# Kernel tuning notes

Hardware: AMD Instinct MI355X
Metric: run time of the kernel (lower is better)

Reference implementation:

```python
import jax, jax.numpy as jnp
import numpy as np

NUM_SEGMENTS = 4096  # number of graphs in the batch


def setup_inputs() -> dict:
    key = jax.random.key(0)
    k1, k2, k3, k4, k5, k6 = jax.random.split(key, 6)
    N, H = 1048576, 128
    x = jax.random.normal(k1, (N, H), dtype=jnp.float32)
    batch = jnp.sort(jax.random.randint(k2, (N,), 0, NUM_SEGMENTS, dtype=jnp.int64))
    # Linear params, PyTorch layout: W [out, in], b [out]
    W1 = jax.random.normal(k3, (2 * H, H), dtype=jnp.float32) * (1.0 / np.sqrt(H))
    b1 = jax.random.normal(k4, (2 * H,), dtype=jnp.float32) * 0.01
    W2 = jax.random.normal(k5, (H, 2 * H), dtype=jnp.float32) * (1.0 / np.sqrt(2 * H))
    b2 = jax.random.normal(k6, (H,), dtype=jnp.float32) * 0.01
    return {"x": x, "batch": batch, "W1": W1, "b1": b1, "W2": W2, "b2": b2}


def reference(x, batch, W1, b1, W2, b2):
    # phi(x) = tanh(fc1(x))  -> [N, 2H]
    phi_x = jnp.tanh(jnp.einsum('nh,oh->no', x, W1) + b1)
    # scatter-sum pooling per graph -> [G, 2H]
    sum_x = jax.ops.segment_sum(phi_x, batch, num_segments=NUM_SEGMENTS)
    # fc2 -> [G, H]; .squeeze() is a no-op for these shapes
    y = jnp.einsum('go,ho->gh', sum_x, W2) + b2
    return jnp.squeeze(y)
```

## Files before the change

### kernel.cpp

```cpp
#include <hip/hip_runtime.h>
#include <hip/hip_bf16.h>

#define NTOT 1048576
#define NSEG 4096
#define HDIM 128
#define ODIM 256
#define GRID1 2048
#define NSTEP 8

typedef __attribute__((ext_vector_type(8))) short bf16x8;
typedef __attribute__((ext_vector_type(4))) float f32x4;
typedef __attribute__((ext_vector_type(4))) unsigned int u32x4;

__device__ __forceinline__ unsigned int cvt_pk(float lo, float hi) {
    unsigned int r;
    asm("v_cvt_pk_bf16_f32 %0, %1, %2" : "=v"(r) : "v"(lo), "v"(hi));
    return r;
}

__global__ void zero_convert(const float* __restrict__ W1, unsigned int* __restrict__ W1b,
                             float* __restrict__ sumx) {
    int gid = blockIdx.x * 256 + threadIdx.x;
    sumx[gid] = 0.0f;
    if (gid < (ODIM * HDIM / 2)) {
        float2 v = *(const float2*)(W1 + 2 * gid);
        W1b[gid] = cvt_pk(v.x, v.y);
    }
}

__global__ __launch_bounds__(256, 2)
void stage1(const float* __restrict__ x, const int* __restrict__ batch,
            const unsigned short* __restrict__ W1b, const float* __restrict__ b1,
            float* __restrict__ sumx) {
    __shared__ __align__(16) unsigned char w1s[ODIM * HDIM * 2];

    const int t    = threadIdx.x;
    const int lane = t & 63;
    const int wv   = t >> 6;
    const int l15  = lane & 15;
    const int lhi  = (lane >> 4) & 3;

    const bool is64 = (batch[NTOT - 1] == 0);

    for (int c = t; c < 4096; c += 256) {
        u32x4 v = ((const u32x4*)W1b)[c];
        int row = c >> 4;
        int kb  = (c & 15) * 16;
        *(u32x4*)(w1s + row * 256 + (kb ^ ((row & 7) << 4))) = v;
    }
    float bias[16];
    #pragma unroll
    for (int nf = 0; nf < 16; ++nf) bias[nf] = b1[nf * 16 + l15];
    __syncthreads();

    int lra[4];
    #pragma unroll
    for (int ks = 0; ks < 4; ++ks)
        lra[ks] = l15 * 256 + ((ks * 64 + lhi * 16) ^ ((l15 & 7) << 4));

    const long rowbase = (long)blockIdx.x * 512 + (long)wv * 128;
    const char* xrow = (const char*)x + (rowbase + l15) * 512 + lhi * 32;

    int curSeg = batch[is64 ? 2 * rowbase : rowbase];
    float runsum[16];
    #pragma unroll
    for (int nf = 0; nf < 16; ++nf) runsum[nf] = 0.f;

#define FLUSH()                                                                  \
    do { if (lhi == 0) {                                                         \
            float* _b = sumx + (long)curSeg * ODIM + l15;                        \
            _Pragma("unroll")                                                    \
            for (int nf = 0; nf < 16; ++nf) atomicAdd(_b + nf * 16, runsum[nf]); \
        }                                                                        \
        _Pragma("unroll")                                                        \
        for (int nf = 0; nf < 16; ++nf) runsum[nf] = 0.f;                        \
    } while (0)

#define LOADSTEP(dst, s)                                                          \
    do { const char* _p = xrow + (size_t)(s) * 8192;                              \
        _Pragma("unroll")                                                         \
        for (int ks = 0; ks < 4; ++ks) {                                          \
            dst[2*ks]   = *(const f32x4*)(_p + ks * 128);                         \
            dst[2*ks+1] = *(const f32x4*)(_p + ks * 128 + 16);                    \
        }                                                                         \
    } while (0)

#define STEP(s, cur, nxt)                                                         \
    do {                                                                          \
        if ((s) + 1 < NSTEP) LOADSTEP(nxt, (s) + 1);    \
        const long _r0 = rowbase + (long)(s) * 16;                                \
        int seg_l = batch[is64 ? 2 * (_r0 + l15) : (_r0 + l15)];                  \
        int prv   = __shfl(seg_l, lane > 0 ? lane - 1 : 0);                       \
        unsigned bm = (unsigned)(__ballot(seg_l != prv)) & 0xFFFEu;               \
        int seg0 = __shfl(seg_l, 0);                                              \
        f32x4 acc[16];                                                            \
        _Pragma("unroll")                                                         \
        for (int nf = 0; nf < 16; ++nf)                                           \
            acc[nf] = (f32x4){bias[nf], bias[nf], bias[nf], bias[nf]};            \
        _Pragma("unroll")                                                         \
        for (int ks = 0; ks < 4; ++ks) {                                          \
            u32x4 w;                                                              \
            w.x = cvt_pk(cur[2*ks].x,   cur[2*ks].y);                             \
            w.y = cvt_pk(cur[2*ks].z,   cur[2*ks].w);                             \
            w.z = cvt_pk(cur[2*ks+1].x, cur[2*ks+1].y);                           \
            w.w = cvt_pk(cur[2*ks+1].z, cur[2*ks+1].w);                           \
            bf16x8 af = __builtin_bit_cast(bf16x8, w);                            \
            _Pragma("unroll")                                                     \
            for (int nf = 0; nf < 16; ++nf) {                                     \
                bf16x8 bf = *(const bf16x8*)(w1s + lra[ks] + nf * 4096);          \
                acc[nf] = __builtin_amdgcn_mfma_f32_16x16x32_bf16(af, bf, acc[nf], 0, 0, 0); \
            }                                                                     \
        }                                                                         \
        _Pragma("unroll")                                                         \
        for (int nf = 0; nf < 16; ++nf)                                           \
            _Pragma("unroll")                                                     \
            for (int r = 0; r < 4; ++r) {                                         \
                float e = exp2f(acc[nf][r] * 2.885390081777927f);                 \
                acc[nf][r] = 1.0f - 2.0f * __builtin_amdgcn_rcpf(1.0f + e);       \
            }                                                                     \
        if (seg0 != curSeg) { FLUSH(); curSeg = seg0; }                           \
        int start = 0;                                                            \
        unsigned rem = bm;                                                        \
        for (;;) {                                                                \
            const int end = rem ? (int)__builtin_ctz(rem) : 16;                   \
            _Pragma("unroll")                                                     \
            for (int nf = 0; nf < 16; ++nf) {                                     \
                float sp = 0.f;                                                   \
                _Pragma("unroll")                                                 \
                for (int r = 0; r < 4; ++r) {                                     \
                    int row = lhi * 4 + r;                                        \
                    float wgt = ((unsigned)(row - start) < (unsigned)(end - start)) ? 1.0f : 0.0f; \
                    sp = fmaf(wgt, acc[nf][r], sp);                               \
                }                                                                 \
                sp += __shfl_xor(sp, 16);                                         \
                sp += __shfl_xor(sp, 32);                                         \
                runsum[nf] += sp;                                                 \
            }                                                                     \
            if (end == 16) break;                                                 \
            FLUSH();                                                              \
            curSeg = __shfl(seg_l, end);                                          \
            rem &= rem - 1;                                                       \
            start = end;                                                          \
        }                                                                         \
    } while (0)

    f32x4 cA[8], cB[8];
    LOADSTEP(cA, 0);
    #pragma unroll
    for (int s = 0; s < NSTEP; s += 2) {
        STEP(s, cA, cB);
        STEP(s + 1, cB, cA);
    }
    FLUSH();

#undef STEP
#undef LOADSTEP
#undef FLUSH
}

__global__ __launch_bounds__(256)
void stage2(const float* __restrict__ sumx, const float* __restrict__ W2,
            const float* __restrict__ b2, float* __restrict__ y) {
    __shared__ float sx[16 * 256];
    const int t = threadIdx.x;
    const long g0 = (long)blockIdx.x * 16;
    #pragma unroll
    for (int i = 0; i < 16; ++i)
        sx[i * 256 + t] = sumx[(g0 + i) * 256 + t];
    __syncthreads();
    const int h = t & 127;
    const int gl0 = (t >> 7) * 8;
    float acc[8] = {0, 0, 0, 0, 0, 0, 0, 0};
    const float* w = W2 + h * 256;
    for (int o4 = 0; o4 < 64; ++o4) {
        float4 wvv = *(const float4*)(w + o4 * 4);
        #pragma unroll
        for (int gl = 0; gl < 8; ++gl) {
            const float* sr = &sx[(gl0 + gl) * 256 + o4 * 4];
            acc[gl] += sr[0] * wvv.x + sr[1] * wvv.y + sr[2] * wvv.z + sr[3] * wvv.w;
        }
    }
    float bb = b2[h];
    #pragma unroll
    for (int gl = 0; gl < 8; ++gl)
        y[(g0 + gl0 + gl) * 128 + h] = acc[gl] + bb;
}

extern "C" void kernel_launch(void* const* d_in, const int* in_sizes, int n_in,
                              void* d_out, int out_size, void* d_ws, size_t ws_size,
                              hipStream_t stream) {
    const float* x   = (const float*)d_in[0];
    const int* batch = (const int*)d_in[1];
    const float* W1  = (const float*)d_in[2];
    const float* b1  = (const float*)d_in[3];
    const float* W2  = (const float*)d_in[4];
    const float* b2  = (const float*)d_in[5];
    float* y = (float*)d_out;

    float* sumx = (float*)d_ws;
    unsigned short* W1b = (unsigned short*)((char*)d_ws + (size_t)NSEG * ODIM * 4);

    zero_convert<<<dim3(NSEG), dim3(256), 0, stream>>>(W1, (unsigned int*)W1b, sumx);
    stage1<<<dim3(GRID1), dim3(256), 0, stream>>>(x, batch, W1b, b1, sumx);
    stage2<<<dim3(NSEG / 16), dim3(256), 0, stream>>>(sumx, W2, b2, y);
}
```

Baseline: 202.0 us.

## Accumulate segment partial sums in shared memory before global atomics

Adds a per-block shared-memory buffer for up to eight segments starting at the block's first segment. Wave flushes now do LDS atomics, and once the block finishes it adds the buffer to global memory with one coalesced pass of atomics, which cuts global atomic traffic and contention. Segment ids for the block's 512 rows are also prefetched into LDS once, replacing the repeated global batch loads. This adds LDS usage, which could lower occupancy, plus an extra barrier and a tail phase of global atomics.

```diff
diff --git a/kernel.cpp b/kernel.cpp
--- a/kernel.cpp
+++ b/kernel.cpp
@@ -7,6 +7,7 @@
 #define ODIM 256
 #define GRID1 2048
 #define NSTEP 8
+#define PSEG 8
 
 typedef __attribute__((ext_vector_type(8))) short bf16x8;
 typedef __attribute__((ext_vector_type(4))) float f32x4;
@@ -33,6 +34,8 @@
             const unsigned short* __restrict__ W1b, const float* __restrict__ b1,
             float* __restrict__ sumx) {
     __shared__ __align__(16) unsigned char w1s[ODIM * HDIM * 2];
+    __shared__ float part[PSEG * ODIM];
+    __shared__ int segAll[512];
 
     const int t    = threadIdx.x;
     const int lane = t & 63;
@@ -41,6 +44,7 @@
     const int lhi  = (lane >> 4) & 3;
 
     const bool is64 = (batch[NTOT - 1] == 0);
+    const long blockrow = (long)blockIdx.x * 512;
 
     for (int c = t; c < 4096; c += 256) {
         u32x4 v = ((const u32x4*)W1b)[c];
@@ -48,9 +52,18 @@
         int kb  = (c & 15) * 16;
         *(u32x4*)(w1s + row * 256 + (kb ^ ((row & 7) << 4))) = v;
     }
+    for (int i = t; i < 512; i += 256) {
+        long idx = blockrow + i;
+        segAll[i] = batch[is64 ? 2 * idx : idx];
+    }
+    for (int i = t; i < PSEG * ODIM; i += 256) part[i] = 0.f;
+
     float bias[16];
     #pragma unroll
     for (int nf = 0; nf < 16; ++nf) bias[nf] = b1[nf * 16 + l15];
+
+    const int segBase = batch[is64 ? 2 * blockrow : blockrow];
+
     __syncthreads();
 
     int lra[4];
@@ -58,22 +71,31 @@
     for (int ks = 0; ks < 4; ++ks)
         lra[ks] = l15 * 256 + ((ks * 64 + lhi * 16) ^ ((l15 & 7) << 4));
 
-    const long rowbase = (long)blockIdx.x * 512 + (long)wv * 128;
+    const long rowbase = blockrow + (long)wv * 128;
     const char* xrow = (const char*)x + (rowbase + l15) * 512 + lhi * 32;
 
-    int curSeg = batch[is64 ? 2 * rowbase : rowbase];
+    int curSeg = segAll[wv * 128];
     float runsum[16];
     #pragma unroll
     for (int nf = 0; nf < 16; ++nf) runsum[nf] = 0.f;
 
-#define FLUSH()                                                                  \
-    do { if (lhi == 0) {                                                         \
-            float* _b = sumx + (long)curSeg * ODIM + l15;                        \
-            _Pragma("unroll")                                                    \
-            for (int nf = 0; nf < 16; ++nf) atomicAdd(_b + nf * 16, runsum[nf]); \
-        }                                                                        \
-        _Pragma("unroll")                                                        \
-        for (int nf = 0; nf < 16; ++nf) runsum[nf] = 0.f;                        \
+#define FLUSH()                                                                   \
+    do { if (lhi == 0) {                                                          \
+            const unsigned _idx = (unsigned)(curSeg - segBase);                   \
+            if (_idx < PSEG) {                                                    \
+                float* _p = &part[_idx * ODIM + l15];                             \
+                _Pragma("unroll")                                                 \
+                for (int nf = 0; nf < 16; ++nf)                                   \
+                    atomicAdd(_p + nf * 16, runsum[nf]);          \
+            } else {                                           \
+                float* _b = sumx + (long)curSeg * ODIM + l15;                     \
+                _Pragma("unroll")                                                 \
+                for (int nf = 0; nf < 16; ++nf)                                   \
+                    atomicAdd(_b + nf * 16, runsum[nf]);                          \
+            }                                                                     \
+        }                                                                         \
+        _Pragma("unroll")                                                         \
+        for (int nf = 0; nf < 16; ++nf) runsum[nf] = 0.f;                         \
     } while (0)
 
 #define LOADSTEP(dst, s)                                                          \
@@ -88,8 +110,7 @@
 #define STEP(s, cur, nxt)                                                         \
     do {                                                                          \
         if ((s) + 1 < NSTEP) LOADSTEP(nxt, (s) + 1);    \
-        const long _r0 = rowbase + (long)(s) * 16;                                \
-        int seg_l = batch[is64 ? 2 * (_r0 + l15) : (_r0 + l15)];                  \
+        int seg_l = segAll[wv * 128 + (s) * 16 + l15];    \
         int prv   = __shfl(seg_l, lane > 0 ? lane - 1 : 0);                       \
         unsigned bm = (unsigned)(__ballot(seg_l != prv)) & 0xFFFEu;               \
         int seg0 = __shfl(seg_l, 0);                                              \
@@ -156,6 +177,13 @@
 #undef STEP
 #undef LOADSTEP
 #undef FLUSH
+
+    __syncthreads();
+    const int segLast = segAll[511];
+    int nrows = segLast - segBase + 1;
+    if (nrows > PSEG) nrows = PSEG;
+    for (int i = t; i < nrows * ODIM; i += 256)
+        atomicAdd(&sumx[(long)(segBase + (i >> 8)) * ODIM + (i & 255)], part[i]);
 }
 
 __global__ __launch_bounds__(256)
```

Result: slower. 216.9 us (+7.4%).
